# Kernel optimization log

Hardware: AMD Instinct MI355X
Metric: run time of the kernel (lower is better)

## Reference

```python
import math
import jax, jax.numpy as jnp
import numpy as np

B, L, D, H = 4, 4096, 1024, 16
DK = D // H


def setup_inputs() -> dict:
    key = jax.random.key(0)
    ks = jax.random.split(key, 11)
    s = 0.02
    return {
        "queries": jax.random.normal(ks[0], (B, L, D), jnp.float32),
        "keys": jax.random.normal(ks[1], (B, L, D), jnp.float32),
        "values": jax.random.normal(ks[2], (B, L, D), jnp.float32),
        "Wq": jax.random.normal(ks[3], (D, D), jnp.float32) * s,
        "bq": jnp.zeros((D,), jnp.float32),
        "Wk": jax.random.normal(ks[4], (D, D), jnp.float32) * s,
        "bk": jnp.zeros((D,), jnp.float32),
        "Wv": jax.random.normal(ks[5], (D, D), jnp.float32) * s,
        "bv": jnp.zeros((D,), jnp.float32),
        "Wo": jax.random.normal(ks[6], (D, D), jnp.float32) * s,
        "bo": jnp.zeros((D,), jnp.float32),
    }


def reference(queries, keys, values, Wq, bq, Wk, bk, Wv, bv, Wo, bo):
    # projections + split heads: (B, H, L, DK)
    q = (queries @ Wq + bq).reshape(B, L, H, DK).transpose(0, 2, 1, 3)
    k = (keys @ Wk + bk).reshape(B, L, H, DK).transpose(0, 2, 1, 3)
    v = (values @ Wv + bv).reshape(B, L, H, DK).transpose(0, 2, 1, 3)

    # per-head mean over channel dim -> (B, H, L)
    qm = q.mean(axis=-1)
    km = k.mean(axis=-1)

    # FFT-based autocorrelation: corr (B, H, L)
    qf = jnp.fft.rfft(qm, axis=-1)
    kf = jnp.fft.rfft(km, axis=-1)
    corr = jnp.fft.irfft(qf * jnp.conj(kf), n=L, axis=-1)

    top_k = max(1, int(math.log(L)))  # top_k=None path -> 8 for L=4096
    w, delays = jax.lax.top_k(corr, top_k)          # (B, H, K)
    w = jax.nn.softmax(w, axis=-1)

    # torch.roll(x, shift=d): out[i] = x[(i - d) mod L]
    pos = jnp.arange(L)
    out = jnp.zeros_like(v)
    for kk in range(top_k):
        idx = (pos[None, None, :] - delays[:, :, kk, None]) % L  # (B, H, L)
        rolled = jnp.take_along_axis(v, idx[..., None], axis=2)  # (B, H, L, DK)
        out = out + w[:, :, kk, None, None] * rolled

    # merge heads (matches per-head concat order) and output projection
    out = out.transpose(0, 2, 1, 3).reshape(B, L, D)
    return out @ Wo + bo
```

## Files before the change

kernel.cpp:

```cpp
#include <hip/hip_runtime.h>
#include <hip/hip_bf16.h>
#include <cstdint>

#define BB 4
#define LL 4096
#define DD 1024
#define HH 16
#define DKH 64
#define MROWS 16384
#define KTOP 8
#define RPB 16

typedef float f32x4 __attribute__((ext_vector_type(4)));
typedef _Float16 f16;
typedef _Float16 f16x4 __attribute__((ext_vector_type(4)));
typedef _Float16 f16x8 __attribute__((ext_vector_type(8)));

__device__ __forceinline__ void gll16(const void* g, void* l) {
    __builtin_amdgcn_global_load_lds(
        (const __attribute__((address_space(1))) void*)g,
        (__attribute__((address_space(3))) void*)l, 16, 0, 0);
}

__global__ void k_colmeans(const float* __restrict__ Wq, const float* __restrict__ bq,
                           const float* __restrict__ Wk, const float* __restrict__ bk,
                           float* __restrict__ Wqm_t, float* __restrict__ Wkm_t,
                           float* __restrict__ bqm, float* __restrict__ bkm) {
    int t = blockIdx.x * blockDim.x + threadIdx.x;
    int which = t >> 14;
    int idx = t & 16383;
    int d = idx >> 4;
    int h = idx & 15;
    const float* W = which ? Wk : Wq;
    const float* p = W + d * DD + h * DKH;
    float s = 0.f;
    #pragma unroll
    for (int c = 0; c < DKH; ++c) s += p[c];
    (which ? Wkm_t : Wqm_t)[h * DD + d] = s * (1.0f / DKH);
    if (d == 0) {
        const float* bb = which ? bk : bq;
        float sb = 0.f;
        for (int c = 0; c < DKH; ++c) sb += bb[h * DKH + c];
        (which ? bkm : bqm)[h] = sb * (1.0f / DKH);
    }
}

__global__ void k_transpose_cvt(const float* __restrict__ in, f16* __restrict__ out) {
    __shared__ float tile[32][33];
    int k0 = blockIdx.x * 32;
    int n0 = blockIdx.y * 32;
    int tx = threadIdx.x, ty = threadIdx.y;
    #pragma unroll
    for (int j = 0; j < 32; j += 8)
        tile[ty + j][tx] = in[(k0 + ty + j) * DD + n0 + tx];
    __syncthreads();
    #pragma unroll
    for (int j = 0; j < 32; j += 8)
        out[(n0 + ty + j) * DD + k0 + tx] = (f16)tile[tx][ty + j];
}

__global__ void k_cvt_f16(const float* __restrict__ in, f16* __restrict__ out) {
    int i = blockIdx.x * blockDim.x + threadIdx.x;
    f32x4 v = ((const f32x4*)in)[i];
    f16x4 o;
    o[0] = (f16)v.x; o[1] = (f16)v.y; o[2] = (f16)v.z; o[3] = (f16)v.w;
    ((f16x4*)out)[i] = o;
}

__global__ __launch_bounds__(256) void k_means(const float* __restrict__ q, const float* __restrict__ k,
                        const float* __restrict__ Wqm_t, const float* __restrict__ Wkm_t,
                        const float* __restrict__ bqm, const float* __restrict__ bkm,
                        float* __restrict__ qm, float* __restrict__ km) {
    __shared__ f32x4 rows4[RPB * 256];
    int isK = blockIdx.x & 1;
    int g = blockIdx.x >> 1;
    const float* src = isK ? k : q;
    const float* W = isK ? Wkm_t : Wqm_t;
    const float* bm = isK ? bkm : bqm;
    float* dst = isK ? km : qm;
    int t = threadIdx.x;
    const f32x4* gsrc = (const f32x4*)src + (size_t)g * (RPB * 256);
    #pragma unroll
    for (int j = 0; j < RPB; ++j) {
        f32x4 v = gsrc[j * 256 + t];
        rows4[j * 256 + (t ^ (j & 7))] = v;
    }
    __syncthreads();
    int rl = t & 15, ks = (t >> 4) & 3, hg = t >> 6;
    int r7 = rl & 7;
    const f32x4* w0 = (const f32x4*)(W + (hg     ) * DD);
    const f32x4* w1 = (const f32x4*)(W + (hg +  4) * DD);
    const f32x4* w2 = (const f32x4*)(W + (hg +  8) * DD);
    const f32x4* w3 = (const f32x4*)(W + (hg + 12) * DD);
    const f32x4* rbase = rows4 + rl * 256;
    float a0 = 0, a1 = 0, a2 = 0, a3 = 0;
    #pragma unroll 4
    for (int i = 0; i < 64; ++i) {
        int c = ks * 64 + i;
        f32x4 r = rbase[c ^ r7];
        f32x4 x0 = w0[c], x1 = w1[c], x2 = w2[c], x3 = w3[c];
        a0 += r.x * x0.x + r.y * x0.y + r.z * x0.z + r.w * x0.w;
        a1 += r.x * x1.x + r.y * x1.y + r.z * x1.z + r.w * x1.w;
        a2 += r.x * x2.x + r.y * x2.y + r.z * x2.z + r.w * x2.w;
        a3 += r.x * x3.x + r.y * x3.y + r.z * x3.z + r.w * x3.w;
    }
    a0 += __shfl_xor(a0, 16); a0 += __shfl_xor(a0, 32);
    a1 += __shfl_xor(a1, 16); a1 += __shfl_xor(a1, 32);
    a2 += __shfl_xor(a2, 16); a2 += __shfl_xor(a2, 32);
    a3 += __shfl_xor(a3, 16); a3 += __shfl_xor(a3, 32);
    if ((t & 48) == 0) {
        int row = g * RPB + rl;
        int b = row >> 12, l = row & 4095;
        dst[((size_t)((b << 4) + hg     ) << 12) + l] = a0 + bm[hg];
        dst[((size_t)((b << 4) + hg +  4) << 12) + l] = a1 + bm[hg + 4];
        dst[((size_t)((b << 4) + hg +  8) << 12) + l] = a2 + bm[hg + 8];
        dst[((size_t)((b << 4) + hg + 12) << 12) + l] = a3 + bm[hg + 12];
    }
}

__global__ __launch_bounds__(1024) void k_corr(const float* __restrict__ qm,
                                               const float* __restrict__ km,
                                               float* __restrict__ corr) {
    __shared__ float sq[LL];
    __shared__ float sk[LL];
    __shared__ f32x4 red[1024];
    int bh = blockIdx.x >> 2;
    int lag0 = (blockIdx.x & 3) * 1024;
    const f32x4* qg = (const f32x4*)(qm + bh * LL);
    const f32x4* kg = (const f32x4*)(km + bh * LL);
    f32x4* sq4 = (f32x4*)sq;
    f32x4* sk4 = (f32x4*)sk;
    int t = threadIdx.x;
    for (int i = t; i < LL / 4; i += 1024) { sq4[i] = qg[i]; sk4[i] = kg[i]; }
    __syncthreads();
    int lt = t & 255;
    int ms = t >> 8;
    int d0 = lag0 + lt * 4;
    int m0 = ms * 1024;
    float a0 = 0, a1 = 0, a2 = 0, a3 = 0;
    f32x4 wv = sq4[((m0 + d0) & 4095) >> 2];
    float w0 = wv.x, w1 = wv.y, w2 = wv.z, w3 = wv.w;
    #pragma unroll 4
    for (int m = m0; m < m0 + 1024; m += 4) {
        f32x4 nx = sq4[((m + 4 + d0) & 4095) >> 2];
        f32x4 kv = sk4[m >> 2];
        a0 += kv.x * w0;  a1 += kv.x * w1;  a2 += kv.x * w2;  a3 += kv.x * w3;
        a0 += kv.y * w1;  a1 += kv.y * w2;  a2 += kv.y * w3;  a3 += kv.y * nx.x;
        a0 += kv.z * w2;  a1 += kv.z * w3;  a2 += kv.z * nx.x; a3 += kv.z * nx.y;
        a0 += kv.w * w3;  a1 += kv.w * nx.x; a2 += kv.w * nx.y; a3 += kv.w * nx.z;
        w0 = nx.x; w1 = nx.y; w2 = nx.z; w3 = nx.w;
    }
    f32x4 p; p.x = a0; p.y = a1; p.z = a2; p.w = a3;
    red[t] = p;
    __syncthreads();
    if (t < 256) {
        f32x4 s0 = red[t], s1 = red[256 + t], s2 = red[512 + t], s3 = red[768 + t];
        f32x4 s;
        s.x = s0.x + s1.x + s2.x + s3.x;
        s.y = s0.y + s1.y + s2.y + s3.y;
        s.z = s0.z + s1.z + s2.z + s3.z;
        s.w = s0.w + s1.w + s2.w + s3.w;
        *(f32x4*)(corr + bh * LL + lag0 + t * 4) = s;
    }
}

__global__ __launch_bounds__(256) void k_topk(const float* __restrict__ corr,
                                              float* __restrict__ wts, int* __restrict__ dls) {
    __shared__ float sc[LL];
    __shared__ float rv[4]; __shared__ int ri[4];
    __shared__ float topv[KTOP]; __shared__ int topi[KTOP];
    int bh = blockIdx.x;
    for (int i = threadIdx.x; i < LL; i += 256) sc[i] = corr[bh * LL + i];
    for (int kk = 0; kk < KTOP; ++kk) {
        __syncthreads();
        float bv = -1e30f; int bi = 0;
        for (int i = threadIdx.x; i < LL; i += 256) {
            float v = sc[i];
            if (v > bv) { bv = v; bi = i; }
        }
        #pragma unroll
        for (int off = 32; off; off >>= 1) {
            float ov = __shfl_down(bv, off);
            int oi = __shfl_down(bi, off);
            if (ov > bv || (ov == bv && oi < bi)) { bv = ov; bi = oi; }
        }
        int wid = threadIdx.x >> 6;
        if ((threadIdx.x & 63) == 0) { rv[wid] = bv; ri[wid] = bi; }
        __syncthreads();
        if (threadIdx.x == 0) {
            for (int w = 1; w < 4; ++w)
                if (rv[w] > bv || (rv[w] == bv && ri[w] < bi)) { bv = rv[w]; bi = ri[w]; }
            topv[kk] = bv; topi[kk] = bi;
            sc[bi] = -1e30f;
        }
    }
    __syncthreads();
    if (threadIdx.x == 0) {
        float mx = topv[0], s = 0.f, e[KTOP];
        #pragma unroll
        for (int kk = 0; kk < KTOP; ++kk) { e[kk] = __expf(topv[kk] - mx); s += e[kk]; }
        float inv = 1.0f / s;
        #pragma unroll
        for (int kk = 0; kk < KTOP; ++kk) {
            wts[bh * KTOP + kk] = e[kk] * inv;
            dls[bh * KTOP + kk] = topi[kk];
        }
    }
}

#define BM 128
#define BN 128
#define BKK 32
template <int MODE>
__global__ __launch_bounds__(256) void k_gemm_bt(const f16* __restrict__ A,
                                                 const f16* __restrict__ BT,
                                                 const float* __restrict__ bias,
                                                 void* __restrict__ Cout) {
    __shared__ f16 As[BM * BKK];
    __shared__ f16 Bs[BN * BKK];
    const int K = DD;
    int n0 = blockIdx.x * BN;
    int m0 = blockIdx.y * BM;
    int tid = threadIdx.x;
    int lane = tid & 63;
    int wave = tid >> 6;
    int wm = wave & 1, wn = wave >> 1;

    int row0 = tid >> 2;
    int slot = tid & 3;
    int kc0 = slot ^ ((row0 >> 1) & 3);
    int row1 = row0 + 64;
    int kc1 = slot ^ ((row1 >> 1) & 3);
    const f16* gA0 = A + (size_t)(m0 + row0) * K + kc0 * 8;
    const f16* gA1 = A + (size_t)(m0 + row1) * K + kc1 * 8;
    const f16* gB0 = BT + (size_t)(n0 + row0) * K + kc0 * 8;
    const f16* gB1 = BT + (size_t)(n0 + row1) * K + kc1 * 8;
    char* ldsA0 = (char*)As + wave * 1024;
    char* ldsA1 = (char*)As + 4096 + wave * 1024;
    char* ldsB0 = (char*)Bs + wave * 1024;
    char* ldsB1 = (char*)Bs + 4096 + wave * 1024;

    int fr = lane & 15;
    int quad = lane >> 4;
    int a_off[4], b_off[4];
    #pragma unroll
    for (int i = 0; i < 4; ++i) {
        int ra = wm * 64 + i * 16 + fr;
        a_off[i] = (ra * 4 + (quad ^ ((ra >> 1) & 3))) * 8;
        int rb = wn * 64 + i * 16 + fr;
        b_off[i] = (rb * 4 + (quad ^ ((rb >> 1) & 3))) * 8;
    }

    f32x4 acc[4][4] = {};
    for (int kt = 0; kt < K; kt += BKK) {
        __syncthreads();
        gll16(gA0, ldsA0);
        gll16(gA1, ldsA1);
        gll16(gB0, ldsB0);
        gll16(gB1, ldsB1);
        gA0 += BKK; gA1 += BKK; gB0 += BKK; gB1 += BKK;
        __syncthreads();
        f16x8 af[4], bf[4];
        #pragma unroll
        for (int i = 0; i < 4; ++i) af[i] = *(const f16x8*)(As + a_off[i]);
        #pragma unroll
        for (int i = 0; i < 4; ++i) bf[i] = *(const f16x8*)(Bs + b_off[i]);
        #pragma unroll
        for (int im = 0; im < 4; ++im)
            #pragma unroll
            for (int in = 0; in < 4; ++in)
                acc[im][in] = __builtin_amdgcn_mfma_f32_16x16x32_f16(af[im], bf[in], acc[im][in], 0, 0, 0);
    }

    #pragma unroll
    for (int in = 0; in < 4; ++in) {
        int col = n0 + wn * 64 + in * 16 + fr;
        float bb = bias[col];
        #pragma unroll
        for (int im = 0; im < 4; ++im) {
            int rowb = m0 + wm * 64 + im * 16 + quad * 4;
            #pragma unroll
            for (int r = 0; r < 4; ++r) {
                float val = acc[im][in][r] + bb;
                if (MODE == 0) {
                    int rr = rowb + r;
                    int b = rr >> 12, l = rr & 4095, h = col >> 6, c = col & 63;
                    ((f16*)Cout)[((size_t)(((b << 4) + h) << 12) + l) * 64 + c] = (f16)val;
                } else {
                    ((float*)Cout)[(size_t)(rowb + r) * DD + col] = val;
                }
            }
        }
    }
}

__global__ __launch_bounds__(256) void k_roll(const f16* __restrict__ V,
                                              const float* __restrict__ wts,
                                              const int* __restrict__ dls,
                                              f16* __restrict__ out) {
    int t = blockIdx.x * 256 + threadIdx.x;
    int cc = t & 7;
    int l = (t >> 3) & 4095;
    int bh = t >> 15;
    const f16* vb = V + ((size_t)bh << 18);
    float a[8] = {};
    #pragma unroll
    for (int kk = 0; kk < KTOP; ++kk) {
        float w = wts[bh * KTOP + kk];
        int d = dls[bh * KTOP + kk];
        int src = (l - d) & 4095;
        f16x8 vv = *(const f16x8*)(vb + (src << 6) + (cc << 3));
        #pragma unroll
        for (int j = 0; j < 8; ++j) a[j] += w * (float)vv[j];
    }
    f16* o = out + ((size_t)((bh >> 4) << 12) + l) * 1024 + ((bh & 15) << 6) + (cc << 3);
    f16x8 ov;
    #pragma unroll
    for (int j = 0; j < 8; ++j) ov[j] = (f16)a[j];
    *(f16x8*)o = ov;
}

extern "C" void kernel_launch(void* const* d_in, const int* in_sizes, int n_in,
                              void* d_out, int out_size, void* d_ws, size_t ws_size,
                              hipStream_t stream) {
    const float* queries = (const float*)d_in[0];
    const float* keys    = (const float*)d_in[1];
    const float* values  = (const float*)d_in[2];
    const float* Wq = (const float*)d_in[3];
    const float* bq = (const float*)d_in[4];
    const float* Wk = (const float*)d_in[5];
    const float* bk = (const float*)d_in[6];
    const float* Wv = (const float*)d_in[7];
    const float* bv = (const float*)d_in[8];
    const float* Wo = (const float*)d_in[9];
    const float* bo = (const float*)d_in[10];

    char* ws = (char*)d_ws;
    size_t off = 0;
    auto alloc = [&](size_t bytes) -> char* {
        char* p = ws + off;
        off += (bytes + 255) & ~(size_t)255;
        return p;
    };
    f16*   values_f16 = (f16*)alloc((size_t)MROWS * DD * 2);
    f16*   Vbuf       = (f16*)alloc((size_t)MROWS * DD * 2);
    f16*   WvT        = (f16*)alloc((size_t)DD * DD * 2);
    f16*   WoT        = (f16*)alloc((size_t)DD * DD * 2);
    float* Wqm_t      = (float*)alloc(HH * DD * 4);
    float* Wkm_t      = (float*)alloc(HH * DD * 4);
    float* bqm        = (float*)alloc(HH * 4);
    float* bkm        = (float*)alloc(HH * 4);
    float* qm         = (float*)alloc((size_t)BB * HH * LL * 4);
    float* km         = (float*)alloc((size_t)BB * HH * LL * 4);
    float* corr       = (float*)alloc((size_t)BB * HH * LL * 4);
    float* wts        = (float*)alloc(BB * HH * KTOP * 4);
    int*   dls        = (int*)alloc(BB * HH * KTOP * 4);
    f16*   out_f16    = values_f16;

    k_colmeans<<<128, 256, 0, stream>>>(Wq, bq, Wk, bk, Wqm_t, Wkm_t, bqm, bkm);
    k_transpose_cvt<<<dim3(32, 32), dim3(32, 8), 0, stream>>>(Wv, WvT);
    k_transpose_cvt<<<dim3(32, 32), dim3(32, 8), 0, stream>>>(Wo, WoT);
    k_cvt_f16<<<16384, 256, 0, stream>>>(values, values_f16);
    k_means<<<2048, 256, 0, stream>>>(queries, keys, Wqm_t, Wkm_t, bqm, bkm, qm, km);
    k_corr<<<256, 1024, 0, stream>>>(qm, km, corr);
    k_topk<<<64, 256, 0, stream>>>(corr, wts, dls);
    k_gemm_bt<0><<<dim3(DD / BN, MROWS / BM), 256, 0, stream>>>(values_f16, WvT, bv, Vbuf);
    k_roll<<<8192, 256, 0, stream>>>(Vbuf, wts, dls, out_f16);
    k_gemm_bt<1><<<dim3(DD / BN, MROWS / BM), 256, 0, stream>>>(out_f16, WoT, bo, d_out);
}
```

Baseline: 475.8 us.

## Restructure k_means to keep weight slices in registers and reduce via butterfly shuffles

Rewrites the head-mean projection kernel so each thread holds a 4-column slice of all 16 head weight rows in registers and streams input rows directly from global memory. The old version staged rows in LDS and re-read weights per row. Per-head partial sums are now combined with a recursive-halving butterfly shuffle reduction, then merged across waves through a small LDS buffer. It also adds an occupancy hint to launch_bounds. This cuts LDS traffic and repeated weight loads, at the cost of higher register pressure from the 64 weight floats held per thread.

```diff
diff --git a/kernel.cpp b/kernel.cpp
--- a/kernel.cpp
+++ b/kernel.cpp
@@ -67,55 +67,68 @@
     ((f16x4*)out)[i] = o;
 }
 
-__global__ __launch_bounds__(256) void k_means(const float* __restrict__ q, const float* __restrict__ k,
+__global__ __launch_bounds__(256, 4) void k_means(const float* __restrict__ q, const float* __restrict__ k,
                         const float* __restrict__ Wqm_t, const float* __restrict__ Wkm_t,
                         const float* __restrict__ bqm, const float* __restrict__ bkm,
                         float* __restrict__ qm, float* __restrict__ km) {
-    __shared__ f32x4 rows4[RPB * 256];
+    __shared__ float lred[RPB * 64];
     int isK = blockIdx.x & 1;
-    int g = blockIdx.x >> 1;
+    int rb  = blockIdx.x >> 1;
     const float* src = isK ? k : q;
-    const float* W = isK ? Wkm_t : Wqm_t;
-    const float* bm = isK ? bkm : bqm;
+    const float* W   = isK ? Wkm_t : Wqm_t;
+    const float* bm  = isK ? bkm : bqm;
     float* dst = isK ? km : qm;
     int t = threadIdx.x;
-    const f32x4* gsrc = (const f32x4*)src + (size_t)g * (RPB * 256);
-    #pragma unroll
-    for (int j = 0; j < RPB; ++j) {
-        f32x4 v = gsrc[j * 256 + t];
-        rows4[j * 256 + (t ^ (j & 7))] = v;
-    }
-    __syncthreads();
-    int rl = t & 15, ks = (t >> 4) & 3, hg = t >> 6;
-    int r7 = rl & 7;
-    const f32x4* w0 = (const f32x4*)(W + (hg     ) * DD);
-    const f32x4* w1 = (const f32x4*)(W + (hg +  4) * DD);
-    const f32x4* w2 = (const f32x4*)(W + (hg +  8) * DD);
-    const f32x4* w3 = (const f32x4*)(W + (hg + 12) * DD);
-    const f32x4* rbase = rows4 + rl * 256;
-    float a0 = 0, a1 = 0, a2 = 0, a3 = 0;
-    #pragma unroll 4
-    for (int i = 0; i < 64; ++i) {
-        int c = ks * 64 + i;
-        f32x4 r = rbase[c ^ r7];
-        f32x4 x0 = w0[c], x1 = w1[c], x2 = w2[c], x3 = w3[c];
-        a0 += r.x * x0.x + r.y * x0.y + r.z * x0.z + r.w * x0.w;
-        a1 += r.x * x1.x + r.y * x1.y + r.z * x1.z + r.w * x1.w;
-        a2 += r.x * x2.x + r.y * x2.y + r.z * x2.z + r.w * x2.w;
-        a3 += r.x * x3.x + r.y * x3.y + r.z * x3.z + r.w * x3.w;
-    }
-    a0 += __shfl_xor(a0, 16); a0 += __shfl_xor(a0, 32);
-    a1 += __shfl_xor(a1, 16); a1 += __shfl_xor(a1, 32);
-    a2 += __shfl_xor(a2, 16); a2 += __shfl_xor(a2, 32);
-    a3 += __shfl_xor(a3, 16); a3 += __shfl_xor(a3, 32);
-    if ((t & 48) == 0) {
-        int row = g * RPB + rl;
-        int b = row >> 12, l = row & 4095;
-        dst[((size_t)((b << 4) + hg     ) << 12) + l] = a0 + bm[hg];
-        dst[((size_t)((b << 4) + hg +  4) << 12) + l] = a1 + bm[hg + 4];
-        dst[((size_t)((b << 4) + hg +  8) << 12) + l] = a2 + bm[hg + 8];
-        dst[((size_t)((b << 4) + hg + 12) << 12) + l] = a3 + bm[hg + 12];
-    }
+    int wavei = t >> 6, lane = t & 63;
+    int c = wavei * 256 + lane * 4;
+    f32x4 wr[16];
+    #pragma unroll
+    for (int h = 0; h < 16; ++h) wr[h] = *(const f32x4*)(W + h * DD + c);
+    const float* rbase = src + (size_t)rb * RPB * DD + c;
+    #pragma unroll 2
+    for (int r = 0; r < RPB; ++r) {
+        f32x4 rv = *(const f32x4*)(rbase + r * DD);
+        float v[16];
+        #pragma unroll
+        for (int h = 0; h < 16; ++h)
+            v[h] = rv.x * wr[h].x + rv.y * wr[h].y + rv.z * wr[h].z + rv.w * wr[h].w;
+        float u[8];
+        #pragma unroll
+        for (int i = 0; i < 8; ++i) {
+            float keep = (lane & 1) ? v[2*i+1] : v[2*i];
+            float send = (lane & 1) ? v[2*i]   : v[2*i+1];
+            u[i] = keep + __shfl_xor(send, 1);
+        }
+        float w2[4];
+        #pragma unroll
+        for (int i = 0; i < 4; ++i) {
+            float keep = (lane & 2) ? u[2*i+1] : u[2*i];
+            float send = (lane & 2) ? u[2*i]   : u[2*i+1];
+            w2[i] = keep + __shfl_xor(send, 2);
+        }
+        float y[2];
+        #pragma unroll
+        for (int i = 0; i < 2; ++i) {
+            float keep = (lane & 4) ? w2[2*i+1] : w2[2*i];
+            float send = (lane & 4) ? w2[2*i]   : w2[2*i+1];
+            y[i] = keep + __shfl_xor(send, 4);
+        }
+        {
+            float keep = (lane & 8) ? y[1] : y[0];
+            float send = (lane & 8) ? y[0] : y[1];
+            float z = keep + __shfl_xor(send, 8);
+            z += __shfl_xor(z, 16);
+            z += __shfl_xor(z, 32);
+            if (lane < 16) lred[r * 64 + wavei * 16 + lane] = z;
+        }
+    }
+    __syncthreads();
+    int rr = t >> 4, h = t & 15;
+    float s = lred[rr * 64 + h] + lred[rr * 64 + 16 + h]
+            + lred[rr * 64 + 32 + h] + lred[rr * 64 + 48 + h] + bm[h];
+    int row = rb * RPB + rr;
+    int b = row >> 12, l = row & 4095;
+    dst[((size_t)((b << 4) + h) << 12) + l] = s;
 }
 
 __global__ __launch_bounds__(1024) void k_corr(const float* __restrict__ qm,
```

Measured after the change: 445.0 us. 1.07x faster.
